# Kernel tuning notes

Hardware: AMD Instinct MI355X
Metric: run time of the kernel (lower is better)

Reference implementation:

```python
import jax, jax.numpy as jnp
import numpy as np

EPS = 1e-5  # BatchNorm eps (eval mode with running stats)

def conv1x1(x, w, b):
    # 1x1x1 Conv3d == channel matmul. x: (b,c,t,h,w), w: (o,c), b: (o,)
    return jnp.einsum('bcthw,oc->bothw', x, w) + b[None, :, None, None, None]

def pool122(x):
    # MaxPool3d kernel (1,2,2): max over non-overlapping 2x2 spatial windows
    b, c, t, h, w = x.shape
    return x.reshape(b, c, t, h // 2, 2, w // 2, 2).max(axis=(4, 6))

def setup_inputs() -> dict:
    key = jax.random.key(0)
    ks = jax.random.split(key, 13)
    C, Ci = 256, 128
    f32 = jnp.float32
    rn = lambda k, s, sc=1.0: jax.random.normal(k, s, dtype=f32) * sc
    return {
        'x': rn(ks[0], (4, C, 8, 32, 32)),
        'g_w': rn(ks[1], (Ci, C), 0.05), 'g_b': rn(ks[2], (Ci,), 0.05),
        'theta_w': rn(ks[3], (Ci, C), 0.05), 'theta_b': rn(ks[4], (Ci,), 0.05),
        'phi_w': rn(ks[5], (Ci, C), 0.05), 'phi_b': rn(ks[6], (Ci,), 0.05),
        'w_w': rn(ks[7], (C, Ci), 0.05), 'w_b': rn(ks[8], (C,), 0.05),
        'bn_gamma': rn(ks[9], (C,), 0.1) + 1.0,
        'bn_beta': rn(ks[10], (C,), 0.1),
        'bn_mean': rn(ks[11], (C,), 0.1),
        'bn_var': jax.random.uniform(ks[12], (C,), dtype=f32, minval=0.5, maxval=1.5),
    }

def reference(x, g_w, g_b, theta_w, theta_b, phi_w, phi_b, w_w, w_b,
              bn_gamma, bn_beta, bn_mean, bn_var):
    b = x.shape[0]
    ci = g_w.shape[0]
    # g, phi: conv then (1,2,2) maxpool (sub_sample=True)
    g_x = pool122(conv1x1(x, g_w, g_b)).reshape(b, ci, -1).transpose(0, 2, 1)      # (b, Nkv, ci)
    theta_x = conv1x1(x, theta_w, theta_b).reshape(b, ci, -1).transpose(0, 2, 1)   # (b, Nq, ci)
    phi_x = pool122(conv1x1(x, phi_w, phi_b)).reshape(b, ci, -1)                    # (b, ci, Nkv)
    f = jnp.einsum('bnc,bcm->bnm', theta_x, phi_x)                                  # (b, Nq, Nkv)
    attn = jax.nn.softmax(f, axis=-1)
    yy = jnp.einsum('bnm,bmc->bnc', attn, g_x)                                      # (b, Nq, ci)
    yy = yy.transpose(0, 2, 1).reshape(b, ci, *x.shape[2:])                         # (b, ci, t, h, w)
    wy = conv1x1(yy, w_w, w_b)
    # BatchNorm3d in eval mode with running stats
    scale = bn_gamma * jax.lax.rsqrt(bn_var + EPS)
    wy = wy * scale[None, :, None, None, None] + (bn_beta - bn_mean * scale)[None, :, None, None, None]
    return wy + x
```

## Files before the change

### kernel.cpp

```cpp
#include <hip/hip_runtime.h>
#include <hip/hip_bf16.h>

typedef __bf16 bf16x8 __attribute__((ext_vector_type(8)));
typedef __bf16 bf16x4 __attribute__((ext_vector_type(4)));
typedef __bf16 bf16x2 __attribute__((ext_vector_type(2)));
typedef float  f32x4  __attribute__((ext_vector_type(4)));
typedef float  f32x2  __attribute__((ext_vector_type(2)));

#define NB   4
#define C_   256
#define CI_  128
#define NSP  8192
#define NKV  2048
#define KVT  32
#define NTH  ((NKV/2)/KVT)
#define NROW (NB*NSP)

__device__ __forceinline__ void gload_lds16(const void* g, void* l) {
    __builtin_amdgcn_global_load_lds(
        (const __attribute__((address_space(1))) void*)(unsigned long long)(uintptr_t)g,
        (__attribute__((address_space(3))) void*)(unsigned)(uintptr_t)l,
        16, 0, 0);
}

__global__ __launch_bounds__(256) void prep_kernel(
    const float* __restrict__ g_w,  const float* __restrict__ g_b,
    const float* __restrict__ th_w, const float* __restrict__ th_b,
    const float* __restrict__ ph_w, const float* __restrict__ ph_b,
    const float* __restrict__ w_w,  const float* __restrict__ w_b,
    const float* __restrict__ bn_g, const float* __restrict__ bn_be,
    const float* __restrict__ bn_m, const float* __restrict__ bn_v,
    __bf16* __restrict__ w_all, __bf16* __restrict__ w2,
    float* __restrict__ b_all, float* __restrict__ bnA, float* __restrict__ bnB)
{
    int idx = blockIdx.x * 256 + threadIdx.x;
    if (idx < 98304) {
        int o = idx >> 8, c = idx & 255;
        float v;
        if (o < 128)      v = th_w[o*256 + c];
        else if (o < 256) v = ph_w[(o-128)*256 + c];
        else              v = g_w[(o-256)*256 + c];
        w_all[idx] = (__bf16)v;
    } else if (idx < 131072) {
        int j = idx - 98304;
        w2[j] = (__bf16)w_w[j];
    } else if (idx < 131456) {
        int k = idx - 131072;
        float v;
        if (k < 128) v = th_b[k]; else if (k < 256) v = ph_b[k-128]; else v = g_b[k-256];
        b_all[k] = v;
    } else if (idx < 131712) {
        int m = idx - 131456;
        float sc = bn_g[m] * rsqrtf(bn_v[m] + 1e-5f);
        bnA[m] = sc;
        bnB[m] = w_b[m]*sc + bn_be[m] - bn_m[m]*sc;
    }
}

__global__ __launch_bounds__(512, 4) void proj_kernel(
    const float* __restrict__ x, const __bf16* __restrict__ w_all,
    const float* __restrict__ b_all,
    __bf16* __restrict__ Q, __bf16* __restrict__ K, __bf16* __restrict__ VT)
{
    __shared__ __bf16 xt[64*256];

    const int b    = blockIdx.x >> 7;
    const int tile = blockIdx.x & 127;
    const int n0   = tile * 64;
    const int tid  = threadIdx.x;
    const int w    = tid >> 6;
    const int lane = tid & 63;
    const int lq   = lane & 15;
    const int g    = lane >> 4;

    const float* xb = x + b * (C_ * NSP);

    {
        const int n = tid & 63;
        const int cw = tid >> 6;
        #pragma unroll
        for (int j = 0; j < 4; ++j) {
            const int cchunk = j*8 + cw;
            const float* xp = xb + (size_t)(cchunk*8)*NSP + n0 + n;
            bf16x8 v;
            #pragma unroll
            for (int e = 0; e < 8; ++e) v[e] = (__bf16)xp[(size_t)e*NSP];
            *(bf16x8*)((char*)xt + n*512 + ((cchunk*16) ^ ((n & 7) << 4))) = v;
        }
    }
    __syncthreads();

    f32x4 acc[4][3];
    #pragma unroll
    for (int a = 0; a < 4; ++a)
        #pragma unroll
        for (int o = 0; o < 3; ++o) acc[a][o] = (f32x4){0.f,0.f,0.f,0.f};

    #pragma unroll 2
    for (int ck = 0; ck < 8; ++ck) {
        const int cbase = ck*32 + g*8;
        bf16x8 afr[4];
        #pragma unroll
        for (int nf = 0; nf < 4; ++nf) {
            const int n = nf*16 + lq;
            afr[nf] = *(const bf16x8*)((const char*)xt + n*512 +
                          ((ck*64 + g*16) ^ ((n & 7) << 4)));
        }
        #pragma unroll
        for (int oi = 0; oi < 3; ++oi) {
            const int orow = (w*3 + oi)*16 + lq;
            bf16x8 bfr = *(const bf16x8*)(w_all + orow*256 + cbase);
            #pragma unroll
            for (int nf = 0; nf < 4; ++nf)
                acc[nf][oi] = __builtin_amdgcn_mfma_f32_16x16x32_bf16(afr[nf], bfr, acc[nf][oi], 0,0,0);
        }
    }

    const int t  = n0 >> 10;
    const int h0 = (n0 & 1023) >> 5;
    const int kvrow0 = t*256 + (h0 >> 1)*16;

    #pragma unroll
    for (int oi = 0; oi < 3; ++oi) {
        const int ocol = (w*3 + oi)*16 + lq;
        const float bias = b_all[ocol];
        float v[4][4];
        #pragma unroll
        for (int nf = 0; nf < 4; ++nf)
            #pragma unroll
            for (int i = 0; i < 4; ++i) v[nf][i] = acc[nf][oi][i] + bias;

        const int seg = ocol >> 7;
        const int ol  = ocol & 127;
        if (seg == 0) {
            #pragma unroll
            for (int nf = 0; nf < 4; ++nf)
                #pragma unroll
                for (int i = 0; i < 4; ++i) {
                    int n = n0 + nf*16 + g*4 + i;
                    Q[(b*NSP + n)*CI_ + ol] = (__bf16)v[nf][i];
                }
        } else if (seg == 1) {
            #pragma unroll
            for (int nfp = 0; nfp < 2; ++nfp)
                #pragma unroll
                for (int j = 0; j < 2; ++j) {
                    float pv = fmaxf(fmaxf(v[nfp][2*j], v[nfp][2*j+1]),
                                     fmaxf(v[nfp+2][2*j], v[nfp+2][2*j+1]));
                    int wp = nfp*8 + g*2 + j;
                    K[(b*NKV + kvrow0 + wp)*CI_ + ol] = (__bf16)pv;
                }
        } else {
            #pragma unroll
            for (int nfp = 0; nfp < 2; ++nfp) {
                bf16x2 pk;
                #pragma unroll
                for (int j = 0; j < 2; ++j) {
                    float pv = fmaxf(fmaxf(v[nfp][2*j], v[nfp][2*j+1]),
                                     fmaxf(v[nfp+2][2*j], v[nfp+2][2*j+1]));
                    pk[j] = (__bf16)pv;
                }
                int wp = nfp*8 + g*2;
                *(bf16x2*)(VT + (b*CI_ + ol)*NKV + kvrow0 + wp) = pk;
            }
        }
    }
}

__global__ __launch_bounds__(256, 2) void attn_kernel(
    const __bf16* __restrict__ Q, const __bf16* __restrict__ K,
    const __bf16* __restrict__ VT, __bf16* __restrict__ o_part,
    float* __restrict__ ml)
{
    __shared__ __bf16 kbuf[3][32*128];
    __shared__ __bf16 vbuf[3][128*32];
    __shared__ __bf16 plds[4][32][40];

    const int b    = blockIdx.x >> 7;
    const int r    = blockIdx.x & 127;
    const int qt   = r >> 1;
    const int kvh  = r & 1;
    const int w    = threadIdx.x >> 6;
    const int lane = threadIdx.x & 63;
    const int lq   = lane & 15;
    const int g    = lane >> 4;
    const int q0   = qt*128 + w*32;
    const int kvbase = kvh * (NKV/2);
    const float LOG2E = 1.4426950408889634f;

    bf16x8 qf[2][4];
    #pragma unroll
    for (int s = 0; s < 2; ++s) {
        const __bf16* qrow = Q + (size_t)(b*NSP + q0 + s*16 + lq)*CI_;
        #pragma unroll
        for (int kk = 0; kk < 4; ++kk) qf[s][kk] = *(const bf16x8*)(qrow + kk*32 + g*8);
    }

    float m_run[2] = {-1e30f, -1e30f}, l_run[2] = {0.f, 0.f};
    f32x4 oacc[2][8];
    #pragma unroll
    for (int s = 0; s < 2; ++s)
        #pragma unroll
        for (int d = 0; d < 8; ++d) oacc[s][d] = (f32x4){0.f,0.f,0.f,0.f};

    const __bf16* Kb0 = K  + (size_t)b*NKV*CI_;
    const __bf16* Vb0 = VT + (size_t)b*CI_*NKV;
    __bf16* pw = &plds[w][0][0];

    auto stage = [&](int bi, int kv0) {
        #pragma unroll
        for (int j = 0; j < 2; ++j) {
            int o   = w*2048 + j*1024 + lane*16;
            int row = o >> 8;
            int c   = (o & 255) ^ ((row & 7) << 4);
            const __bf16* src = Kb0 + (size_t)(kv0 + row)*CI_ + (c >> 1);
            gload_lds16(src, (char*)&kbuf[bi][0] + w*2048 + j*1024);
        }
        #pragma unroll
        for (int j = 0; j < 2; ++j) {
            int o    = w*2048 + j*1024 + lane*16;
            int row  = o >> 6;
            int slot = (o >> 4) & 3;
            int kc   = slot ^ ((row >> 1) & 3);
            const __bf16* src = Vb0 + (size_t)row*NKV + kv0 + kc*8;
            gload_lds16(src, (char*)&vbuf[bi][0] + w*2048 + j*1024);
        }
    };

    stage(0, kvbase);
    stage(1, kvbase + KVT);

    for (int t = 0; t < NTH; ++t) {
        asm volatile("s_waitcnt vmcnt(4)" ::: "memory");
        __builtin_amdgcn_s_barrier();
        __builtin_amdgcn_sched_barrier(0);

        {
            int tn = t + 2;
            int kvn = kvbase + (tn < NTH ? tn : NTH-1) * KVT;
            stage(tn % 3, kvn);
        }

        const int bi = t % 3;
        const char* kb = (const char*)&kbuf[bi][0];
        const char* vb = (const char*)&vbuf[bi][0];

        f32x4 facc[2][2];
        #pragma unroll
        for (int s = 0; s < 2; ++s)
            #pragma unroll
            for (int nf = 0; nf < 2; ++nf) facc[s][nf] = (f32x4){0.f,0.f,0.f,0.f};
        __builtin_amdgcn_s_setprio(1);
        #pragma unroll
        for (int kk = 0; kk < 4; ++kk) {
            #pragma unroll
            for (int nf = 0; nf < 2; ++nf) {
                int row = nf*16 + lq;
                int c   = (kk*64 + g*16) ^ ((row & 7) << 4);
                bf16x8 kf = *(const bf16x8*)(kb + row*256 + c);
                facc[0][nf] = __builtin_amdgcn_mfma_f32_16x16x32_bf16(kf, qf[0][kk], facc[0][nf], 0,0,0);
                facc[1][nf] = __builtin_amdgcn_mfma_f32_16x16x32_bf16(kf, qf[1][kk], facc[1][nf], 0,0,0);
            }
        }
        __builtin_amdgcn_s_setprio(0);

        #pragma unroll
        for (int s = 0; s < 2; ++s) {
            float m0 = fmaxf(fmaxf(facc[s][0][0], facc[s][0][1]), fmaxf(facc[s][0][2], facc[s][0][3]));
            float m1 = fmaxf(fmaxf(facc[s][1][0], facc[s][1][1]), fmaxf(facc[s][1][2], facc[s][1][3]));
            float pmax = fmaxf(m0, m1);
            pmax = fmaxf(pmax, __shfl_xor(pmax, 16, 64));
            pmax = fmaxf(pmax, __shfl_xor(pmax, 32, 64));
            if (!__all(pmax - m_run[s] <= 8.f)) {
                float mnew = fmaxf(m_run[s], pmax);
                float corr = __builtin_amdgcn_exp2f((m_run[s] - mnew) * LOG2E);
                l_run[s] *= corr;
                #pragma unroll
                for (int d = 0; d < 8; ++d) {
                    oacc[s][d][0] *= corr; oacc[s][d][1] *= corr;
                    oacc[s][d][2] *= corr; oacc[s][d][3] *= corr;
                }
                m_run[s] = mnew;
            }
            float p[8];
            #pragma unroll
            for (int nf = 0; nf < 2; ++nf)
                #pragma unroll
                for (int i = 0; i < 4; ++i)
                    p[nf*4+i] = __builtin_amdgcn_exp2f((facc[s][nf][i] - m_run[s]) * LOG2E);
            float ps = ((p[0]+p[1]) + (p[2]+p[3])) + ((p[4]+p[5]) + (p[6]+p[7]));
            ps += __shfl_xor(ps, 16, 64);
            ps += __shfl_xor(ps, 32, 64);
            l_run[s] += ps;
            #pragma unroll
            for (int nf = 0; nf < 2; ++nf) {
                bf16x4 pk;
                #pragma unroll
                for (int i = 0; i < 4; ++i) pk[i] = (__bf16)p[nf*4+i];
                *(bf16x4*)(pw + (s*16 + lq)*40 + nf*16 + g*4) = pk;
            }
        }
        bf16x8 pb[2];
        #pragma unroll
        for (int s = 0; s < 2; ++s)
            pb[s] = *(const bf16x8*)(pw + (s*16 + lq)*40 + g*8);

        __builtin_amdgcn_s_setprio(1);
        #pragma unroll
        for (int df = 0; df < 8; ++df) {
            int row = df*16 + lq;
            int cb  = (g*16) ^ (((row >> 1) & 3) << 4);
            bf16x8 vf = *(const bf16x8*)(vb + row*64 + cb);
            oacc[0][df] = __builtin_amdgcn_mfma_f32_16x16x32_bf16(vf, pb[0], oacc[0][df], 0,0,0);
            oacc[1][df] = __builtin_amdgcn_mfma_f32_16x16x32_bf16(vf, pb[1], oacc[1][df], 0,0,0);
        }
        __builtin_amdgcn_s_setprio(0);
    }

    #pragma unroll
    for (int s = 0; s < 2; ++s) {
        const int row = b*NSP + q0 + s*16 + lq;
        __bf16* orow = o_part + ((size_t)kvh*NROW + row)*CI_;
        #pragma unroll
        for (int df = 0; df < 8; ++df) {
            bf16x4 ov;
            #pragma unroll
            for (int i = 0; i < 4; ++i) ov[i] = (__bf16)oacc[s][df][i];
            *(bf16x4*)(orow + df*16 + g*4) = ov;
        }
        if (g == 0) {
            f32x2 v; v[0] = m_run[s]; v[1] = l_run[s];
            *(f32x2*)(ml + ((size_t)kvh*NROW + row)*2) = v;
        }
    }
}

__global__ __launch_bounds__(256, 4) void out_kernel(
    const __bf16* __restrict__ o_part, const float* __restrict__ ml,
    const __bf16* __restrict__ w2,
    const float* __restrict__ bnA, const float* __restrict__ bnB,
    const float* __restrict__ x, float* __restrict__ out)
{
    const int b    = blockIdx.x >> 8;
    const int tile = blockIdx.x & 255;
    const int n0   = tile * 32;
    const int w    = threadIdx.x >> 6;
    const int lane = threadIdx.x & 63;
    const int lq   = lane & 15;
    const int g    = lane >> 4;
    const float LOG2E = 1.4426950408889634f;

    float c1[2], c2[2];
    #pragma unroll
    for (int nf = 0; nf < 2; ++nf) {
        const size_t row = (size_t)b*NSP + n0 + nf*16 + lq;
        f32x2 ml1 = *(const f32x2*)(ml + row*2);
        f32x2 ml2 = *(const f32x2*)(ml + (NROW + row)*2);
        float M  = fmaxf(ml1[0], ml2[0]);
        float e1 = __builtin_amdgcn_exp2f((ml1[0] - M) * LOG2E);
        float e2 = __builtin_amdgcn_exp2f((ml2[0] - M) * LOG2E);
        float dinv = 1.f / (e1*ml1[1] + e2*ml2[1]);
        c1[nf] = e1 * dinv;
        c2[nf] = e2 * dinv;
    }

    f32x4 acc[4][2];
    #pragma unroll
    for (int a = 0; a < 4; ++a)
        #pragma unroll
        for (int o = 0; o < 2; ++o) acc[a][o] = (f32x4){0.f,0.f,0.f,0.f};

    #pragma unroll
    for (int kk = 0; kk < 4; ++kk) {
        bf16x8 afr[2];
        #pragma unroll
        for (int nf = 0; nf < 2; ++nf) {
            const size_t off = ((size_t)b*NSP + n0 + nf*16 + lq)*CI_ + kk*32 + g*8;
            bf16x8 o1 = *(const bf16x8*)(o_part + off);
            bf16x8 o2 = *(const bf16x8*)(o_part + (size_t)NROW*CI_ + off);
            bf16x8 af;
            #pragma unroll
            for (int e = 0; e < 8; ++e)
                af[e] = (__bf16)(c1[nf]*(float)o1[e] + c2[nf]*(float)o2[e]);
            afr[nf] = af;
        }
        #pragma unroll
        for (int cf = 0; cf < 4; ++cf) {
            const int corow = (w*4 + cf)*16 + lq;
            bf16x8 bfr = *(const bf16x8*)(w2 + corow*CI_ + kk*32 + g*8);
            #pragma unroll
            for (int nf = 0; nf < 2; ++nf)
                acc[cf][nf] = __builtin_amdgcn_mfma_f32_16x16x32_bf16(afr[nf], bfr, acc[cf][nf], 0,0,0);
        }
    }

    #pragma unroll
    for (int cf = 0; cf < 4; ++cf) {
        const int co = (w*4 + cf)*16 + lq;
        const float A = bnA[co], Bv = bnB[co];
        #pragma unroll
        for (int nf = 0; nf < 2; ++nf) {
            const int n = n0 + nf*16 + g*4;
            size_t idx = (size_t)(b*C_ + co)*NSP + n;
            f32x4 xv = *(const f32x4*)(x + idx);
            f32x4 ov;
            #pragma unroll
            for (int i = 0; i < 4; ++i) ov[i] = acc[cf][nf][i]*A + Bv + xv[i];
            *(f32x4*)(out + idx) = ov;
        }
    }
}

extern "C" void kernel_launch(void* const* d_in, const int* in_sizes, int n_in,
                              void* d_out, int out_size, void* d_ws, size_t ws_size,
                              hipStream_t stream)
{
    const float* x    = (const float*)d_in[0];
    const float* g_w  = (const float*)d_in[1];
    const float* g_b  = (const float*)d_in[2];
    const float* th_w = (const float*)d_in[3];
    const float* th_b = (const float*)d_in[4];
    const float* ph_w = (const float*)d_in[5];
    const float* ph_b = (const float*)d_in[6];
    const float* w_w  = (const float*)d_in[7];
    const float* w_b  = (const float*)d_in[8];
    const float* bn_g = (const float*)d_in[9];
    const float* bn_be= (const float*)d_in[10];
    const float* bn_m = (const float*)d_in[11];
    const float* bn_v = (const float*)d_in[12];

    char* ws = (char*)d_ws;
    size_t off = 0;
    auto alloc = [&](size_t bytes) -> void* {
        void* p = ws + off;
        off += (bytes + 255) & ~(size_t)255;
        return p;
    };
    __bf16* w_all = (__bf16*)alloc(384*256*2);
    __bf16* w2    = (__bf16*)alloc(256*128*2);
    float*  b_all = (float*) alloc(384*4);
    float*  bnA   = (float*) alloc(256*4);
    float*  bnB   = (float*) alloc(256*4);
    __bf16* Qb    = (__bf16*)alloc((size_t)NROW*CI_*2);
    __bf16* Kb    = (__bf16*)alloc((size_t)NB*NKV*CI_*2);
    __bf16* Vt    = (__bf16*)alloc((size_t)NB*CI_*NKV*2);
    __bf16* oPart = (__bf16*)alloc((size_t)2*NROW*CI_*2);
    float*  mlB   = (float*) alloc((size_t)2*NROW*2*4);

    prep_kernel<<<515, 256, 0, stream>>>(g_w, g_b, th_w, th_b, ph_w, ph_b, w_w, w_b,
                                         bn_g, bn_be, bn_m, bn_v,
                                         w_all, w2, b_all, bnA, bnB);
    proj_kernel<<<512, 512, 0, stream>>>(x, w_all, b_all, Qb, Kb, Vt);
    attn_kernel<<<512, 256, 0, stream>>>(Qb, Kb, Vt, oPart, mlB);
    out_kernel <<<1024, 256, 0, stream>>>(oPart, mlB, w2, bnA, bnB, x, (float*)d_out);
}
```

Baseline: 194.9 us.

## Fuse four kernels into one cooperative persistent kernel with grid syncs

Replaces the prep, projection, attention and output launches with a single cooperative kernel of 512 blocks that runs each stage in turn, separated by grid-wide barriers. The goal is to remove per-launch overhead and the gaps between kernels. In exchange every stage must fit a 256-thread block and shared launch bounds, which changes occupancy and tiling for some stages (the projection stage drops from 512 to 256 threads per block). The grid syncs also add their own cost, and the old four-kernel path remains as a fallback if the cooperative launch is unavailable.

```diff
diff --git a/kernel.cpp b/kernel.cpp
--- a/kernel.cpp
+++ b/kernel.cpp
@@ -1,5 +1,8 @@
 #include <hip/hip_runtime.h>
 #include <hip/hip_bf16.h>
+#include <hip/hip_cooperative_groups.h>
+
+namespace cg = cooperative_groups;
 
 typedef __bf16 bf16x8 __attribute__((ext_vector_type(8)));
 typedef __bf16 bf16x4 __attribute__((ext_vector_type(4)));
@@ -21,6 +24,394 @@
         (const __attribute__((address_space(1))) void*)(unsigned long long)(uintptr_t)g,
         (__attribute__((address_space(3))) void*)(unsigned)(uintptr_t)l,
         16, 0, 0);
+}
+
+__global__ __launch_bounds__(256, 2) void fused_kernel(
+    const float* __restrict__ x,
+    const float* __restrict__ g_w,  const float* __restrict__ g_b,
+    const float* __restrict__ th_w, const float* __restrict__ th_b,
+    const float* __restrict__ ph_w, const float* __restrict__ ph_b,
+    const float* __restrict__ w_w,  const float* __restrict__ w_b,
+    const float* __restrict__ bn_g, const float* __restrict__ bn_be,
+    const float* __restrict__ bn_m, const float* __restrict__ bn_v,
+    __bf16* __restrict__ w_all, __bf16* __restrict__ w2,
+    float* __restrict__ b_all, float* __restrict__ bnA, float* __restrict__ bnB,
+    __bf16* __restrict__ Q, __bf16* __restrict__ K, __bf16* __restrict__ VT,
+    __bf16* __restrict__ o_part, float* __restrict__ ml,
+    float* __restrict__ out)
+{
+    __shared__ __align__(16) char smem[59392];
+    cg::grid_group grid = cg::this_grid();
+
+    const int bid  = blockIdx.x;
+    const int tid  = threadIdx.x;
+    const int lane = tid & 63;
+    const int w    = tid >> 6;
+    const int lq   = lane & 15;
+    const int g    = lane >> 4;
+    const float LOG2E = 1.4426950408889634f;
+
+    {
+        const int idx0 = bid*256 + tid;
+        #pragma unroll
+        for (int r = 0; r < 2; ++r) {
+            int idx = idx0 + r*131072;
+            if (idx < 98304) {
+                int o = idx >> 8, c = idx & 255;
+                float v;
+                if (o < 128)      v = th_w[o*256 + c];
+                else if (o < 256) v = ph_w[(o-128)*256 + c];
+                else              v = g_w[(o-256)*256 + c];
+                w_all[idx] = (__bf16)v;
+            } else if (idx < 131072) {
+                int j = idx - 98304;
+                w2[j] = (__bf16)w_w[j];
+            } else if (idx < 131456) {
+                int k = idx - 131072;
+                float v;
+                if (k < 128) v = th_b[k]; else if (k < 256) v = ph_b[k-128]; else v = g_b[k-256];
+                b_all[k] = v;
+            } else if (idx < 131712) {
+                int m = idx - 131456;
+                float sc = bn_g[m] * rsqrtf(bn_v[m] + 1e-5f);
+                bnA[m] = sc;
+                bnB[m] = w_b[m]*sc + bn_be[m] - bn_m[m]*sc;
+            }
+        }
+    }
+    __threadfence();
+    grid.sync();
+    __threadfence();
+
+    {
+        __bf16* xt = (__bf16*)smem;
+        const int b    = bid >> 7;
+        const int tile = bid & 127;
+        const int n0   = tile * 64;
+        const float* xb = x + b * (C_ * NSP);
+
+        const int n  = tid & 63;
+        const int cw = tid >> 6;
+        #pragma unroll
+        for (int j = 0; j < 8; ++j) {
+            const int cchunk = j*4 + cw;
+            const float* xp = xb + (size_t)(cchunk*8)*NSP + n0 + n;
+            bf16x8 v;
+            #pragma unroll
+            for (int e = 0; e < 8; ++e) v[e] = (__bf16)xp[(size_t)e*NSP];
+            *(bf16x8*)((char*)xt + n*512 + ((cchunk*16) ^ ((n & 7) << 4))) = v;
+        }
+        __syncthreads();
+
+        f32x4 acc[4][6];
+        #pragma unroll
+        for (int a = 0; a < 4; ++a)
+            #pragma unroll
+            for (int o = 0; o < 6; ++o) acc[a][o] = (f32x4){0.f,0.f,0.f,0.f};
+
+        #pragma unroll 2
+        for (int ck = 0; ck < 8; ++ck) {
+            const int cbase = ck*32 + g*8;
+            bf16x8 afr[4];
+            #pragma unroll
+            for (int nf = 0; nf < 4; ++nf) {
+                const int n2 = nf*16 + lq;
+                afr[nf] = *(const bf16x8*)((const char*)xt + n2*512 +
+                              ((ck*64 + g*16) ^ ((n2 & 7) << 4)));
+            }
+            #pragma unroll
+            for (int oi = 0; oi < 6; ++oi) {
+                const int orow = (w*6 + oi)*16 + lq;
+                bf16x8 bfr = *(const bf16x8*)(w_all + orow*256 + cbase);
+                #pragma unroll
+                for (int nf = 0; nf < 4; ++nf)
+                    acc[nf][oi] = __builtin_amdgcn_mfma_f32_16x16x32_bf16(afr[nf], bfr, acc[nf][oi], 0,0,0);
+            }
+        }
+
+        const int t  = n0 >> 10;
+        const int h0 = (n0 & 1023) >> 5;
+        const int kvrow0 = t*256 + (h0 >> 1)*16;
+
+        #pragma unroll
+        for (int oi = 0; oi < 6; ++oi) {
+            const int ocol = (w*6 + oi)*16 + lq;
+            const float bias = b_all[ocol];
+            float v[4][4];
+            #pragma unroll
+            for (int nf = 0; nf < 4; ++nf)
+                #pragma unroll
+                for (int i = 0; i < 4; ++i) v[nf][i] = acc[nf][oi][i] + bias;
+
+            const int seg = ocol >> 7;
+            const int ol  = ocol & 127;
+            if (seg == 0) {
+                #pragma unroll
+                for (int nf = 0; nf < 4; ++nf)
+                    #pragma unroll
+                    for (int i = 0; i < 4; ++i) {
+                        int nn = n0 + nf*16 + g*4 + i;
+                        Q[(b*NSP + nn)*CI_ + ol] = (__bf16)v[nf][i];
+                    }
+            } else if (seg == 1) {
+                #pragma unroll
+                for (int nfp = 0; nfp < 2; ++nfp)
+                    #pragma unroll
+                    for (int j = 0; j < 2; ++j) {
+                        float pv = fmaxf(fmaxf(v[nfp][2*j], v[nfp][2*j+1]),
+                                         fmaxf(v[nfp+2][2*j], v[nfp+2][2*j+1]));
+                        int wp = nfp*8 + g*2 + j;
+                        K[(b*NKV + kvrow0 + wp)*CI_ + ol] = (__bf16)pv;
+                    }
+            } else {
+                #pragma unroll
+                for (int nfp = 0; nfp < 2; ++nfp) {
+                    bf16x2 pk;
+                    #pragma unroll
+                    for (int j = 0; j < 2; ++j) {
+                        float pv = fmaxf(fmaxf(v[nfp][2*j], v[nfp][2*j+1]),
+                                         fmaxf(v[nfp+2][2*j], v[nfp+2][2*j+1]));
+                        pk[j] = (__bf16)pv;
+                    }
+                    int wp = nfp*8 + g*2;
+                    *(bf16x2*)(VT + (b*CI_ + ol)*NKV + kvrow0 + wp) = pk;
+                }
+            }
+        }
+    }
+    __threadfence();
+    grid.sync();
+    __threadfence();
+
+    {
+        __bf16* kbufB = (__bf16*)smem;
+        __bf16* vbufB = (__bf16*)(smem + 24576);
+        __bf16* plds  = (__bf16*)(smem + 49152);
+
+        const int b    = bid >> 7;
+        const int r    = bid & 127;
+        const int qt   = r >> 1;
+        const int kvh  = r & 1;
+        const int q0   = qt*128 + w*32;
+        const int kvbase = kvh * (NKV/2);
+
+        bf16x8 qf[2][4];
+        #pragma unroll
+        for (int s = 0; s < 2; ++s) {
+            const __bf16* qrow = Q + (size_t)(b*NSP + q0 + s*16 + lq)*CI_;
+            #pragma unroll
+            for (int kk = 0; kk < 4; ++kk) qf[s][kk] = *(const bf16x8*)(qrow + kk*32 + g*8);
+        }
+        asm volatile("s_waitcnt vmcnt(0)" ::: "memory");
+
+        float m_run[2] = {-1e30f, -1e30f}, l_run[2] = {0.f, 0.f};
+        f32x4 oacc[2][8];
+        #pragma unroll
+        for (int s = 0; s < 2; ++s)
+            #pragma unroll
+            for (int d = 0; d < 8; ++d) oacc[s][d] = (f32x4){0.f,0.f,0.f,0.f};
+
+        const __bf16* Kb0 = K  + (size_t)b*NKV*CI_;
+        const __bf16* Vb0 = VT + (size_t)b*CI_*NKV;
+        __bf16* pw = plds + w*(32*40);
+
+        auto stage = [&](int bi, int kv0) {
+            #pragma unroll
+            for (int j = 0; j < 2; ++j) {
+                int o   = w*2048 + j*1024 + lane*16;
+                int row = o >> 8;
+                int c   = (o & 255) ^ ((row & 7) << 4);
+                const __bf16* src = Kb0 + (size_t)(kv0 + row)*CI_ + (c >> 1);
+                gload_lds16(src, (char*)kbufB + bi*8192 + w*2048 + j*1024);
+            }
+            #pragma unroll
+            for (int j = 0; j < 2; ++j) {
+                int o    = w*2048 + j*1024 + lane*16;
+                int row  = o >> 6;
+                int slot = (o >> 4) & 3;
+                int kc   = slot ^ ((row >> 1) & 3);
+                const __bf16* src = Vb0 + (size_t)row*NKV + kv0 + kc*8;
+                gload_lds16(src, (char*)vbufB + bi*8192 + w*2048 + j*1024);
+            }
+        };
+
+        stage(0, kvbase);
+        stage(1, kvbase + KVT);
+
+        for (int t = 0; t < NTH; ++t) {
+            asm volatile("s_waitcnt vmcnt(4)" ::: "memory");
+            __builtin_amdgcn_s_barrier();
+            __builtin_amdgcn_sched_barrier(0);
+
+            {
+                int tn = t + 2;
+                int kvn = kvbase + (tn < NTH ? tn : NTH-1) * KVT;
+                stage(tn % 3, kvn);
+            }
+
+            const int bi = t % 3;
+            const char* kb = (const char*)kbufB + bi*8192;
+            const char* vb = (const char*)vbufB + bi*8192;
+
+            f32x4 facc[2][2];
+            #pragma unroll
+            for (int s = 0; s < 2; ++s)
+                #pragma unroll
+                for (int nf = 0; nf < 2; ++nf) facc[s][nf] = (f32x4){0.f,0.f,0.f,0.f};
+            __builtin_amdgcn_s_setprio(1);
+            #pragma unroll
+            for (int kk = 0; kk < 4; ++kk) {
+                #pragma unroll
+                for (int nf = 0; nf < 2; ++nf) {
+                    int row = nf*16 + lq;
+                    int c   = (kk*64 + g*16) ^ ((row & 7) << 4);
+                    bf16x8 kf = *(const bf16x8*)(kb + row*256 + c);
+                    facc[0][nf] = __builtin_amdgcn_mfma_f32_16x16x32_bf16(kf, qf[0][kk], facc[0][nf], 0,0,0);
+                    facc[1][nf] = __builtin_amdgcn_mfma_f32_16x16x32_bf16(kf, qf[1][kk], facc[1][nf], 0,0,0);
+                }
+            }
+            __builtin_amdgcn_s_setprio(0);
+
+            #pragma unroll
+            for (int s = 0; s < 2; ++s) {
+                float m0 = fmaxf(fmaxf(facc[s][0][0], facc[s][0][1]), fmaxf(facc[s][0][2], facc[s][0][3]));
+                float m1 = fmaxf(fmaxf(facc[s][1][0], facc[s][1][1]), fmaxf(facc[s][1][2], facc[s][1][3]));
+                float pmax = fmaxf(m0, m1);
+                pmax = fmaxf(pmax, __shfl_xor(pmax, 16, 64));
+                pmax = fmaxf(pmax, __shfl_xor(pmax, 32, 64));
+                if (!__all(pmax - m_run[s] <= 8.f)) {
+                    float mnew = fmaxf(m_run[s], pmax);
+                    float corr = __builtin_amdgcn_exp2f((m_run[s] - mnew) * LOG2E);
+                    l_run[s] *= corr;
+                    #pragma unroll
+                    for (int d = 0; d < 8; ++d) {
+                        oacc[s][d][0] *= corr; oacc[s][d][1] *= corr;
+                        oacc[s][d][2] *= corr; oacc[s][d][3] *= corr;
+                    }
+                    m_run[s] = mnew;
+                }
+                float p[8];
+                #pragma unroll
+                for (int nf = 0; nf < 2; ++nf)
+                    #pragma unroll
+                    for (int i = 0; i < 4; ++i)
+                        p[nf*4+i] = __builtin_amdgcn_exp2f((facc[s][nf][i] - m_run[s]) * LOG2E);
+                float ps = ((p[0]+p[1]) + (p[2]+p[3])) + ((p[4]+p[5]) + (p[6]+p[7]));
+                ps += __shfl_xor(ps, 16, 64);
+                ps += __shfl_xor(ps, 32, 64);
+                l_run[s] += ps;
+                #pragma unroll
+                for (int nf = 0; nf < 2; ++nf) {
+                    bf16x4 pk;
+                    #pragma unroll
+                    for (int i = 0; i < 4; ++i) pk[i] = (__bf16)p[nf*4+i];
+                    *(bf16x4*)(pw + (s*16 + lq)*40 + nf*16 + g*4) = pk;
+                }
+            }
+            bf16x8 pb[2];
+            #pragma unroll
+            for (int s = 0; s < 2; ++s)
+                pb[s] = *(const bf16x8*)(pw + (s*16 + lq)*40 + g*8);
+
+            __builtin_amdgcn_s_setprio(1);
+            #pragma unroll
+            for (int df = 0; df < 8; ++df) {
+                int row = df*16 + lq;
+                int cb  = (g*16) ^ (((row >> 1) & 3) << 4);
+                bf16x8 vf = *(const bf16x8*)(vb + row*64 + cb);
+                oacc[0][df] = __builtin_amdgcn_mfma_f32_16x16x32_bf16(vf, pb[0], oacc[0][df], 0,0,0);
+                oacc[1][df] = __builtin_amdgcn_mfma_f32_16x16x32_bf16(vf, pb[1], oacc[1][df], 0,0,0);
+            }
+            __builtin_amdgcn_s_setprio(0);
+        }
+
+        #pragma unroll
+        for (int s = 0; s < 2; ++s) {
+            const int row = b*NSP + q0 + s*16 + lq;
+            __bf16* orow = o_part + ((size_t)kvh*NROW + row)*CI_;
+            #pragma unroll
+            for (int df = 0; df < 8; ++df) {
+                bf16x4 ov;
+                #pragma unroll
+                for (int i = 0; i < 4; ++i) ov[i] = (__bf16)oacc[s][df][i];
+                *(bf16x4*)(orow + df*16 + g*4) = ov;
+            }
+            if (g == 0) {
+                f32x2 v; v[0] = m_run[s]; v[1] = l_run[s];
+                *(f32x2*)(ml + ((size_t)kvh*NROW + row)*2) = v;
+            }
+        }
+    }
+    __threadfence();
+    grid.sync();
+    __threadfence();
+
+    #pragma unroll 1
+    for (int rep = 0; rep < 2; ++rep) {
+        const int tile2 = bid*2 + rep;
+        const int b     = tile2 >> 8;
+        const int n0    = (tile2 & 255) * 32;
+
+        float c1[2], c2[2];
+        #pragma unroll
+        for (int nf = 0; nf < 2; ++nf) {
+            const size_t row = (size_t)b*NSP + n0 + nf*16 + lq;
+            f32x2 ml1 = *(const f32x2*)(ml + row*2);
+            f32x2 ml2 = *(const f32x2*)(ml + (NROW + row)*2);
+            float M  = fmaxf(ml1[0], ml2[0]);
+            float e1 = __builtin_amdgcn_exp2f((ml1[0] - M) * LOG2E);
+            float e2 = __builtin_amdgcn_exp2f((ml2[0] - M) * LOG2E);
+            float dinv = 1.f / (e1*ml1[1] + e2*ml2[1]);
+            c1[nf] = e1 * dinv;
+            c2[nf] = e2 * dinv;
+        }
+
+        f32x4 acc[4][2];
+        #pragma unroll
+        for (int a = 0; a < 4; ++a)
+            #pragma unroll
+            for (int o = 0; o < 2; ++o) acc[a][o] = (f32x4){0.f,0.f,0.f,0.f};
+
+        #pragma unroll
+        for (int kk = 0; kk < 4; ++kk) {
+            bf16x8 afr[2];
+            #pragma unroll
+            for (int nf = 0; nf < 2; ++nf) {
+                const size_t off = ((size_t)b*NSP + n0 + nf*16 + lq)*CI_ + kk*32 + g*8;
+                bf16x8 o1 = *(const bf16x8*)(o_part + off);
+                bf16x8 o2 = *(const bf16x8*)(o_part + (size_t)NROW*CI_ + off);
+                bf16x8 af;
+                #pragma unroll
+                for (int e = 0; e < 8; ++e)
+                    af[e] = (__bf16)(c1[nf]*(float)o1[e] + c2[nf]*(float)o2[e]);
+                afr[nf] = af;
+            }
+            #pragma unroll
+            for (int cf = 0; cf < 4; ++cf) {
+                const int corow = (w*4 + cf)*16 + lq;
+                bf16x8 bfr = *(const bf16x8*)(w2 + corow*CI_ + kk*32 + g*8);
+                #pragma unroll
+                for (int nf = 0; nf < 2; ++nf)
+                    acc[cf][nf] = __builtin_amdgcn_mfma_f32_16x16x32_bf16(afr[nf], bfr, acc[cf][nf], 0,0,0);
+            }
+        }
+
+        #pragma unroll
+        for (int cf = 0; cf < 4; ++cf) {
+            const int co = (w*4 + cf)*16 + lq;
+            const float A = bnA[co], Bv = bnB[co];
+            #pragma unroll
+            for (int nf = 0; nf < 2; ++nf) {
+                const int n = n0 + nf*16 + g*4;
+                size_t idx = (size_t)(b*C_ + co)*NSP + n;
+                f32x4 xv = *(const f32x4*)(x + idx);
+                f32x4 ov;
+                #pragma unroll
+                for (int i = 0; i < 4; ++i) ov[i] = acc[cf][nf][i]*A + Bv + xv[i];
+                *(f32x4*)(out + idx) = ov;
+            }
+        }
+    }
 }
 
 __global__ __launch_bounds__(256) void prep_kernel(
@@ -446,11 +837,37 @@
     __bf16* Vt    = (__bf16*)alloc((size_t)NB*CI_*NKV*2);
     __bf16* oPart = (__bf16*)alloc((size_t)2*NROW*CI_*2);
     float*  mlB   = (float*) alloc((size_t)2*NROW*2*4);
-
-    prep_kernel<<<515, 256, 0, stream>>>(g_w, g_b, th_w, th_b, ph_w, ph_b, w_w, w_b,
-                                         bn_g, bn_be, bn_m, bn_v,
-                                         w_all, w2, b_all, bnA, bnB);
-    proj_kernel<<<512, 512, 0, stream>>>(x, w_all, b_all, Qb, Kb, Vt);
-    attn_kernel<<<512, 256, 0, stream>>>(Qb, Kb, Vt, oPart, mlB);
-    out_kernel <<<1024, 256, 0, stream>>>(oPart, mlB, w2, bnA, bnB, x, (float*)d_out);
+    float*  outp  = (float*)d_out;
+
+    int dev = 0;
+    (void)hipGetDevice(&dev);
+    int coopSupported = 0;
+    (void)hipDeviceGetAttribute(&coopSupported, hipDeviceAttributeCooperativeLaunch, dev);
+    int occ = 0;
+    (void)hipOccupancyMaxActiveBlocksPerMultiprocessor(&occ, (const void*)fused_kernel, 256, 0);
+
+    hipError_t st = hipErrorUnknown;
+    if (coopSupported && occ >= 2) {
+        void* kargs[] = {
+            (void*)&x,
+            (void*)&g_w,  (void*)&g_b,
+            (void*)&th_w, (void*)&th_b,
+            (void*)&ph_w, (void*)&ph_b,
+            (void*)&w_w,  (void*)&w_b,
+            (void*)&bn_g, (void*)&bn_be, (void*)&bn_m, (void*)&bn_v,
+            (void*)&w_all, (void*)&w2, (void*)&b_all, (void*)&bnA, (void*)&bnB,
+            (void*)&Qb, (void*)&Kb, (void*)&Vt, (void*)&oPart, (void*)&mlB,
+            (void*)&outp
+        };
+        st = hipLaunchCooperativeKernel((void*)fused_kernel, dim3(512), dim3(256),
+                                        kargs, 0, stream);
+    }
+    if (st != hipSuccess) {
+        prep_kernel<<<515, 256, 0, stream>>>(g_w, g_b, th_w, th_b, ph_w, ph_b, w_w, w_b,
+                                             bn_g, bn_be, bn_m, bn_v,
+                                             w_all, w2, b_all, bnA, bnB);
+        proj_kernel<<<512, 512, 0, stream>>>(x, w_all, b_all, Qb, Kb, Vt);
+        attn_kernel<<<512, 256, 0, stream>>>(Qb, Kb, Vt, oPart, mlB);
+        out_kernel <<<1024, 256, 0, stream>>>(oPart, mlB, w2, bnA, bnB, x, outp);
+    }
 }
```

Measured after the change: 195.5 us. Within noise of the previous version (+0.3%).
